# Kernel tuning notes

Measured on AMD Instinct MI355X. Metric: run time of the kernel, lower is better.

The kernel has to match this reference:

```python
import jax, jax.numpy as jnp
import numpy as np

N = 20000
E = 320000
R1 = 8        # num_rels (layer 1)
R2 = 256      # layer-2 num_rels == out_size (faithful to original positional-arg bug)
B = 8         # num_bases
D = 256       # hid_size == out_size
TIME_DIM = 2880
POI_DIM = 12
ROAD_DIM = 32


def relconv(h, src, dst, etype, coeff, bases, loop_w, bias):
    """DGL RelGraphConv with basis regularizer, sum aggregation, self-loop, bias.
    W_r = sum_b coeff[r,b] * bases[b]; msg_e = h[src_e] @ W_{etype_e}; agg = scatter-add to dst.
    Implemented memory-efficiently: project nodes into basis space once [B,N,D],
    then scan over the B bases (small fixed loop) for the gather/scale/scatter.
    """
    tb = jnp.einsum('nd,bdo->bno', h, bases)          # [B, N, D]
    c = coeff[etype]                                   # [E, B] per-edge basis coeffs

    def body(agg, xs):
        tb_b, c_b = xs                                 # [N,D], [E]
        msg = c_b[:, None] * tb_b[src]                 # [E, D]
        return agg + jax.ops.segment_sum(msg, dst, num_segments=N), None

    agg0 = jnp.zeros((N, bases.shape[-1]), h.dtype)
    agg, _ = jax.lax.scan(body, agg0, (tb, c.T))
    return agg + h @ loop_w + bias


def rgcn2(feat, src, dst, etype, c1, v1, l1, b1, c2, v2, l2, b2):
    h = relconv(feat, src, dst, etype, c1, v1, l1, b1)
    h = jax.nn.relu(h)  # dropout p=0.0 -> identity
    h = relconv(h, src, dst, etype, c2, v2, l2, b2)
    return h


def setup_inputs() -> dict:
    key = jax.random.key(0)
    ks = iter(jax.random.split(key, 48))
    f32 = jnp.float32

    def nrm(shape, std=0.02):
        return (jax.random.normal(next(ks), shape, dtype=f32) * std)

    inp = {
        'poi_distribution': jax.random.uniform(next(ks), (N, POI_DIM), dtype=f32),
        'time_distribution': jax.random.normal(next(ks), (N, TIME_DIM), dtype=f32),
        'road_feature': jax.random.normal(next(ks), (N, ROAD_DIM), dtype=f32),
        # input projections (torch Linear: stored here as [in,out])
        'W_poi': nrm((POI_DIM, 64)), 'b_poi': jnp.zeros((64,), f32),
        'W_time': nrm((TIME_DIM, 128)), 'b_time': jnp.zeros((128,), f32),
        'W_road': nrm((ROAD_DIM, 64)), 'b_road': jnp.zeros((64,), f32),
        # adj R-GCN layer params: coeff [R,B], bases [B,D,D], loop [D,D], bias [D]
        'a_coeff1': nrm((R1, B), 0.3), 'a_bases1': nrm((B, D, D)),
        'a_loop1': nrm((D, D)), 'a_bias1': jnp.zeros((D,), f32),
        'a_coeff2': nrm((R2, B), 0.3), 'a_bases2': nrm((B, D, D)),
        'a_loop2': nrm((D, D)), 'a_bias2': jnp.zeros((D,), f32),
        # no_adj R-GCN layer params
        'n_coeff1': nrm((R1, B), 0.3), 'n_bases1': nrm((B, D, D)),
        'n_loop1': nrm((D, D)), 'n_bias1': jnp.zeros((D,), f32),
        'n_coeff2': nrm((R2, B), 0.3), 'n_bases2': nrm((B, D, D)),
        'n_loop2': nrm((D, D)), 'n_bias2': jnp.zeros((D,), f32),
        # fusion
        'W_fuse': nrm((D, D)), 'b_fuse': jnp.zeros((D,), f32),
        'W_fuse_kg': nrm((D, D)), 'b_fuse_kg': jnp.zeros((D,), f32),
        # graphs (edge lists + relation types)
        'adj_src': jax.random.randint(next(ks), (E,), 0, N, dtype=jnp.int32),
        'adj_dst': jax.random.randint(next(ks), (E,), 0, N, dtype=jnp.int32),
        'adj_type': jax.random.randint(next(ks), (E,), 0, R1, dtype=jnp.int32),
        'no_adj_src': jax.random.randint(next(ks), (E,), 0, N, dtype=jnp.int32),
        'no_adj_dst': jax.random.randint(next(ks), (E,), 0, N, dtype=jnp.int32),
        'no_adj_type': jax.random.randint(next(ks), (E,), 0, R1, dtype=jnp.int32),
    }
    return inp


def reference(poi_distribution, time_distribution, road_feature,
              W_poi, b_poi, W_time, b_time, W_road, b_road,
              a_coeff1, a_bases1, a_loop1, a_bias1,
              a_coeff2, a_bases2, a_loop2, a_bias2,
              n_coeff1, n_bases1, n_loop1, n_bias1,
              n_coeff2, n_bases2, n_loop2, n_bias2,
              W_fuse, b_fuse, W_fuse_kg, b_fuse_kg,
              adj_src, adj_dst, adj_type,
              no_adj_src, no_adj_dst, no_adj_type):
    poi_feat = poi_distribution @ W_poi + b_poi       # [N, 64]
    time_feat = time_distribution @ W_time + b_time   # [N, 128]
    road_feat = road_feature @ W_road + b_road        # [N, 64]
    feat = jnp.concatenate([poi_feat, time_feat, road_feat], axis=1)  # [N, 256]

    adj_emb = rgcn2(feat, adj_src, adj_dst, adj_type,
                    a_coeff1, a_bases1, a_loop1, a_bias1,
                    a_coeff2, a_bases2, a_loop2, a_bias2)
    no_adj_emb = rgcn2(feat, no_adj_src, no_adj_dst, no_adj_type,
                       n_coeff1, n_bases1, n_loop1, n_bias1,
                       n_coeff2, n_bases2, n_loop2, n_bias2)

    fused = (adj_emb @ W_fuse + b_fuse) + (no_adj_emb @ W_fuse_kg + b_fuse_kg)
    return jax.nn.gelu(fused, approximate=False)      # torch nn.GELU is exact erf
```

## Files before the change

kernel.cpp:

```cpp
#include <hip/hip_runtime.h>
#include <math.h>

typedef unsigned short ushort_t;
typedef __bf16 bf16x8 __attribute__((ext_vector_type(8)));
typedef float  f32x4  __attribute__((ext_vector_type(4)));

constexpr int NN = 20000;
constexpr int EE = 320000;
constexpr int NC = 2304;
constexpr int TD = 2880;

__device__ __forceinline__ float b2f(ushort_t u) {
    return __uint_as_float(((unsigned int)u) << 16);
}
__device__ __forceinline__ ushort_t f2b(float f) {
    unsigned int u = __float_as_uint(f);
    u += 0x7fffu + ((u >> 16) & 1u);
    return (ushort_t)(u >> 16);
}
__device__ __forceinline__ float ldf(const void* p, size_t i, int f32m) {
    return f32m ? ((const float*)p)[i] : b2f(((const ushort_t*)p)[i]);
}
__device__ __forceinline__ void gl2lds16(const ushort_t* g, ushort_t* l) {
    __builtin_amdgcn_global_load_lds(
        (const __attribute__((address_space(1))) void*)g,
        (__attribute__((address_space(3))) void*)l, 16, 0, 0);
}

__device__ __forceinline__ void mfma_step(const ushort_t* As, const ushort_t* Bs,
                                          f32x4 (&acc)[4][4],
                                          int wm, int wn, int quad, int l16)
{
    bf16x8 afr[4], bfr[4];
#pragma unroll
    for (int mi = 0; mi < 4; mi++)
        afr[mi] = *(const bf16x8*)(As + (wm * 64 + mi * 16 + l16) * 32 + quad * 8);
#pragma unroll
    for (int ni = 0; ni < 4; ni++)
        bfr[ni] = *(const bf16x8*)(Bs + (wn * 64 + ni * 16 + l16) * 32 + quad * 8);
#pragma unroll
    for (int mi = 0; mi < 4; mi++)
#pragma unroll
        for (int ni = 0; ni < 4; ni++)
            acc[mi][ni] = __builtin_amdgcn_mfma_f32_16x16x32_bf16(
                afr[mi], bfr[ni], acc[mi][ni], 0, 0, 0);
}

__global__ void k_detect(const void* timeD, int* flags)
{
    __shared__ float mx[256];
    int t = threadIdx.x;
    float m = 0.f;
    for (int i = t; i < 1024; i += 256) {
        float v = fabsf(b2f(((const ushort_t*)timeD)[i]));
        if (!(v < 1e30f)) v = 1e30f;
        m = fmaxf(m, v);
    }
    mx[t] = m;
    __syncthreads();
    if (t == 0) {
        float mm = 0.f;
        for (int i = 0; i < 256; i++) mm = fmaxf(mm, mx[i]);
        flags[0] = (mm > 1e4f) ? 1 : 0;
        flags[1] = 0;
    }
}

__global__ void k_cvt16(const void* __restrict__ in, ushort_t* __restrict__ out,
                        int n, const int* __restrict__ mf)
{
    int f32m = mf[0];
    int i = blockIdx.x * 256 + threadIdx.x;
    if (i < n) out[i] = f32m ? f2b(((const float*)in)[i]) : ((const ushort_t*)in)[i];
}

__global__ __launch_bounds__(256) void gemm_bt(
    const ushort_t* __restrict__ A, int lda,
    const ushort_t* __restrict__ Bt, int ldb,
    void* __restrict__ C, int ldc, int col0, const int* __restrict__ of,
    const ushort_t* __restrict__ bias,
    int M, int Ncols, int K, int act)
{
    __shared__ ushort_t As[128 * 32];
    __shared__ ushort_t Bs[128 * 32];

    const int f32o = of[0];
    const int t    = threadIdx.x;
    const int wave = t >> 6, lane = t & 63;
    const int wm   = wave >> 1, wn = wave & 1;
    const int quad = lane >> 4, l16 = lane & 15;
    const int m0   = blockIdx.x * 128, n0 = blockIdx.y * 128;

    f32x4 acc[4][4];
#pragma unroll
    for (int i = 0; i < 4; i++)
#pragma unroll
        for (int j = 0; j < 4; j++) acc[i][j] = (f32x4){0.f, 0.f, 0.f, 0.f};

    for (int k0 = 0; k0 < K; k0 += 32) {
#pragma unroll
        for (int j = 0; j < 2; j++) {
            int c   = (wave * 2 + j) * 64 + lane;
            int row = c >> 2, kc = c & 3;
            ushort_t* ldsbase_a = As + (wave * 2 + j) * 512;
            ushort_t* ldsbase_b = Bs + (wave * 2 + j) * 512;
            gl2lds16(A  + (size_t)(m0 + row) * lda + k0 + kc * 8, ldsbase_a);
            gl2lds16(Bt + (size_t)(n0 + row) * ldb + k0 + kc * 8, ldsbase_b);
        }
        __syncthreads();
        mfma_step(As, Bs, acc, wm, wn, quad, l16);
        __syncthreads();
    }

#pragma unroll
    for (int mi = 0; mi < 4; mi++) {
#pragma unroll
        for (int r = 0; r < 4; r++) {
            int row = m0 + wm * 64 + mi * 16 + quad * 4 + r;
            if (row >= M) continue;
#pragma unroll
            for (int ni = 0; ni < 4; ni++) {
                int col = n0 + wn * 64 + ni * 16 + l16;
                float v = acc[mi][ni][r];
                if (bias) v += b2f(bias[col]);
                if (act == 1) v = fmaxf(v, 0.f);
                else if (act == 2) v = 0.5f * v * (1.f + erff(v * 0.70710678118654752f));
                size_t idx = (size_t)row * ldc + col0 + col;
                if (f32o) ((float*)C)[idx] = v;
                else      ((ushort_t*)C)[idx] = f2b(v);
            }
        }
    }
}

__global__ __launch_bounds__(256) void gemm_splitk(
    const void* __restrict__ A, int lda, const int* __restrict__ af,
    const ushort_t* __restrict__ Bt, int ldb,
    float* __restrict__ part, int M, int K, int KC)
{
    __shared__ ushort_t As[128 * 32];
    __shared__ ushort_t Bs[128 * 32];

    const int f32a = af[0];
    const int t    = threadIdx.x;
    const int wave = t >> 6, lane = t & 63;
    const int wm   = wave >> 1, wn = wave & 1;
    const int quad = lane >> 4, l16 = lane & 15;
    const int m0   = blockIdx.x * 128;
    const int kbeg = blockIdx.y * KC;
    const int kend = (kbeg + KC < K) ? kbeg + KC : K;

    f32x4 acc[4][4];
#pragma unroll
    for (int i = 0; i < 4; i++)
#pragma unroll
        for (int j = 0; j < 4; j++) acc[i][j] = (f32x4){0.f, 0.f, 0.f, 0.f};

    if (!f32a && (m0 + 128 <= M)) {
        const ushort_t* Ab = (const ushort_t*)A;
        for (int k0 = kbeg; k0 < kend; k0 += 32) {
#pragma unroll
            for (int j = 0; j < 2; j++) {
                int c   = (wave * 2 + j) * 64 + lane;
                int row = c >> 2, kc = c & 3;
                gl2lds16(Ab + (size_t)(m0 + row) * lda + k0 + kc * 8,
                         As + (wave * 2 + j) * 512);
                gl2lds16(Bt + (size_t)row * ldb + k0 + kc * 8,
                         Bs + (wave * 2 + j) * 512);
            }
            __syncthreads();
            mfma_step(As, Bs, acc, wm, wn, quad, l16);
            __syncthreads();
        }
    } else {
        for (int k0 = kbeg; k0 < kend; k0 += 32) {
#pragma unroll
            for (int i = 0; i < 2; i++) {
                int c = t + i * 256;
                int row = c >> 2, kc = c & 3;
                uint4 av = make_uint4(0, 0, 0, 0);
                int gr = m0 + row;
                if (gr < M) {
                    size_t base = (size_t)gr * lda + k0 + kc * 8;
                    if (f32a) {
                        const float* Af = (const float*)A + base;
                        float4 lo = *(const float4*)Af;
                        float4 hi = *(const float4*)(Af + 4);
                        av.x = (unsigned)f2b(lo.x) | ((unsigned)f2b(lo.y) << 16);
                        av.y = (unsigned)f2b(lo.z) | ((unsigned)f2b(lo.w) << 16);
                        av.z = (unsigned)f2b(hi.x) | ((unsigned)f2b(hi.y) << 16);
                        av.w = (unsigned)f2b(hi.z) | ((unsigned)f2b(hi.w) << 16);
                    } else {
                        av = *(const uint4*)((const ushort_t*)A + base);
                    }
                }
                *(uint4*)(As + row * 32 + kc * 8) = av;
                uint4 bv = *(const uint4*)(Bt + (size_t)row * ldb + k0 + kc * 8);
                *(uint4*)(Bs + row * 32 + kc * 8) = bv;
            }
            __syncthreads();
            mfma_step(As, Bs, acc, wm, wn, quad, l16);
            __syncthreads();
        }
    }

    float* dst = part + (size_t)blockIdx.y * ((size_t)M * 128);
#pragma unroll
    for (int mi = 0; mi < 4; mi++) {
#pragma unroll
        for (int r = 0; r < 4; r++) {
            int row = m0 + wm * 64 + mi * 16 + quad * 4 + r;
            if (row >= M) continue;
#pragma unroll
            for (int ni = 0; ni < 4; ni++) {
                int col = wn * 64 + ni * 16 + l16;
                dst[(size_t)row * 128 + col] = acc[mi][ni][r];
            }
        }
    }
}

__global__ void k_bias_time(const float* __restrict__ part, int nsplit,
                            const ushort_t* __restrict__ bt,
                            ushort_t* __restrict__ feat)
{
    int n = blockIdx.x, o = threadIdx.x;
    float a = b2f(bt[o]);
    for (int s = 0; s < nsplit; ++s)
        a += part[(size_t)s * NN * 128 + (size_t)n * 128 + o];
    feat[(size_t)n * 256 + 64 + o] = f2b(a);
}

__global__ void k_build_wcatT(const void* __restrict__ coeff,
                              const void* __restrict__ bases,
                              const void* __restrict__ loopw,
                              ushort_t* __restrict__ Wt, const int* __restrict__ mf)
{
    __shared__ ushort_t tile[32][33];
    int f32m = mf[0];
    int blk = blockIdx.x;
    int r = blk >> 6, kt = (blk >> 3) & 7, ot = blk & 7;
    int k0 = kt * 32, o0 = ot * 32;
    int oi = threadIdx.x & 31, k4 = threadIdx.x >> 5;
    float cf[8];
    if (r < 8) {
#pragma unroll
        for (int b = 0; b < 8; b++) cf[b] = ldf(coeff, r * 8 + b, f32m);
    }
#pragma unroll
    for (int p = 0; p < 4; ++p) {
        int ki = k4 * 4 + p, k = k0 + ki, o = o0 + oi;
        float acc;
        if (r == 8) {
            acc = ldf(loopw, (size_t)k * 256 + o, f32m);
        } else {
            acc = 0.f;
#pragma unroll
            for (int b = 0; b < 8; b++)
                acc += cf[b] * ldf(bases, ((size_t)b * 256 + k) * 256 + o, f32m);
        }
        tile[ki][oi] = f2b(acc);
    }
    __syncthreads();
    int ki2 = threadIdx.x & 31, o4 = threadIdx.x >> 5;
#pragma unroll
    for (int p = 0; p < 4; ++p) {
        int o2 = o4 * 4 + p;
        Wt[((size_t)(r * 256 + o0 + o2)) * 256 + k0 + ki2] = tile[ki2][o2];
    }
}

__global__ void k_trans32(const void* __restrict__ in, ushort_t* __restrict__ out,
                          int cols, int ldout, const int* __restrict__ mf)
{
    __shared__ ushort_t tile[32][33];
    int f32m = mf[0];
    int k0 = blockIdx.x * 32, o0 = blockIdx.y * 32;
    int oi = threadIdx.x & 31, k4 = threadIdx.x >> 5;
#pragma unroll
    for (int p = 0; p < 4; ++p) {
        int ki = k4 * 4 + p;
        tile[ki][oi] = f2b(ldf(in, (size_t)(k0 + ki) * cols + (o0 + oi), f32m));
    }
    __syncthreads();
    int ki2 = threadIdx.x & 31, o4 = threadIdx.x >> 5;
#pragma unroll
    for (int p = 0; p < 4; ++p) {
        int o2 = o4 * 4 + p;
        out[(size_t)(o0 + o2) * ldout + k0 + ki2] = tile[ki2][o2];
    }
}

__global__ void k_biasfuse(const void* __restrict__ bf, const void* __restrict__ bfk,
                           ushort_t* __restrict__ bias_cat, const int* __restrict__ mf)
{
    int f32m = mf[0];
    int o = threadIdx.x;
    bias_cat[o] = f2b(ldf(bf, o, f32m) + ldf(bfk, o, f32m));
}

__global__ void k_inproj(const void* __restrict__ poi, const void* __restrict__ Wp,
                         const void* __restrict__ bp,
                         const void* __restrict__ road, const void* __restrict__ Wr,
                         const void* __restrict__ br,
                         ushort_t* __restrict__ feat, const int* __restrict__ mf)
{
    int f32m = mf[0];
    int n = blockIdx.x, t = threadIdx.x;
    if (t < 64) {
        float a = ldf(bp, t, f32m);
#pragma unroll
        for (int k = 0; k < 12; k++)
            a += ldf(poi, (size_t)n * 12 + k, f32m) * ldf(Wp, k * 64 + t, f32m);
        feat[(size_t)n * 256 + t] = f2b(a);
    } else {
        int o = t - 64;
        float a = ldf(br, o, f32m);
#pragma unroll
        for (int k = 0; k < 32; k++)
            a += ldf(road, (size_t)n * 32 + k, f32m) * ldf(Wr, k * 64 + o, f32m);
        feat[(size_t)n * 256 + 192 + o] = f2b(a);
    }
}

__global__ void k_zero(int* __restrict__ p, int n)
{
    int i = blockIdx.x * 256 + threadIdx.x;
    if (i < n) p[i] = 0;
}
__global__ void k_count(const int* __restrict__ dst, int* __restrict__ deg, int e)
{
    int i = blockIdx.x * 256 + threadIdx.x;
    if (i < e) atomicAdd(&deg[dst[i]], 1);
}
__global__ void k_scan1(const int* __restrict__ deg, int* __restrict__ partial,
                        int* __restrict__ bsum, int n)
{
    int t = threadIdx.x, b = blockIdx.x;
    int i = b * 256 + t;
    int v = (i < n) ? deg[i] : 0;
    int lane = t & 63, w = t >> 6;
    int x = v;
#pragma unroll
    for (int d = 1; d < 64; d <<= 1) {
        int y = __shfl_up(x, d);
        if (lane >= d) x += y;
    }
    __shared__ int wt[4];
    if (lane == 63) wt[w] = x;
    __syncthreads();
    int woff = 0;
    for (int j = 0; j < 4; j++) if (j < w) woff += wt[j];
    int incl = x + woff;
    if (i < n) partial[i] = incl - v;
    if (t == 255) bsum[b] = incl;
}
__global__ void k_scan2(const int* __restrict__ bsum, int* __restrict__ boff, int nb)
{
    int t = threadIdx.x;
    int v = (t < nb) ? bsum[t] : 0;
    int lane = t & 63, w = t >> 6;
    int x = v;
#pragma unroll
    for (int d = 1; d < 64; d <<= 1) {
        int y = __shfl_up(x, d);
        if (lane >= d) x += y;
    }
    __shared__ int wt[4];
    if (lane == 63) wt[w] = x;
    __syncthreads();
    int woff = 0;
    for (int j = 0; j < 4; j++) if (j < w) woff += wt[j];
    boff[t] = (x + woff) - v;
}
__global__ void k_scan3(const int* __restrict__ boff, int* __restrict__ rs,
                        int* __restrict__ cur, int n)
{
    int i = blockIdx.x * 256 + threadIdx.x;
    if (i < n) {
        int v = rs[i] + boff[blockIdx.x];
        rs[i] = v;
        cur[i] = v;
    }
}
__global__ void k_fill(const int* __restrict__ src, const int* __restrict__ dst,
                       const int* __restrict__ et, int* __restrict__ cur,
                       int* __restrict__ sorted, int e)
{
    int i = blockIdx.x * 256 + threadIdx.x;
    if (i < e) {
        int pos = atomicAdd(&cur[dst[i]], 1);
        sorted[pos] = (src[i] << 3) | et[i];
    }
}

__global__ __launch_bounds__(256) void k_agg_full(
    const ushort_t* __restrict__ tb,
    const int* __restrict__ rs, const int* __restrict__ deg,
    const int* __restrict__ sorted, const ushort_t* __restrict__ bias,
    ushort_t* __restrict__ out, int ldo, int col0, int act, int n_nodes)
{
    int w = blockIdx.x * 4 + (threadIdx.x >> 6);
    if (w >= n_nodes) return;
    int lane = threadIdx.x & 63;
    int lo = lane * 4;

    float a0 = b2f(bias[lo + 0]);
    float a1 = b2f(bias[lo + 1]);
    float a2 = b2f(bias[lo + 2]);
    float a3 = b2f(bias[lo + 3]);
    {
        ushort4 lv = *(const ushort4*)(tb + (size_t)w * NC + 8 * 256 + lo);
        a0 += b2f(lv.x); a1 += b2f(lv.y); a2 += b2f(lv.z); a3 += b2f(lv.w);
    }
    int s = rs[w], cnt = deg[w];
    int j = 0;
    for (; j + 4 <= cnt; j += 4) {
        int p0 = sorted[s + j + 0];
        int p1 = sorted[s + j + 1];
        int p2 = sorted[s + j + 2];
        int p3 = sorted[s + j + 3];
        ushort4 v0 = *(const ushort4*)(tb + ((size_t)(p0 >> 3) * 9 + (p0 & 7)) * 256 + lo);
        ushort4 v1 = *(const ushort4*)(tb + ((size_t)(p1 >> 3) * 9 + (p1 & 7)) * 256 + lo);
        ushort4 v2 = *(const ushort4*)(tb + ((size_t)(p2 >> 3) * 9 + (p2 & 7)) * 256 + lo);
        ushort4 v3 = *(const ushort4*)(tb + ((size_t)(p3 >> 3) * 9 + (p3 & 7)) * 256 + lo);
        a0 += b2f(v0.x); a1 += b2f(v0.y); a2 += b2f(v0.z); a3 += b2f(v0.w);
        a0 += b2f(v1.x); a1 += b2f(v1.y); a2 += b2f(v1.z); a3 += b2f(v1.w);
        a0 += b2f(v2.x); a1 += b2f(v2.y); a2 += b2f(v2.z); a3 += b2f(v2.w);
        a0 += b2f(v3.x); a1 += b2f(v3.y); a2 += b2f(v3.z); a3 += b2f(v3.w);
    }
    for (; j < cnt; ++j) {
        int p = sorted[s + j];
        ushort4 v = *(const ushort4*)(tb + ((size_t)(p >> 3) * 9 + (p & 7)) * 256 + lo);
        a0 += b2f(v.x); a1 += b2f(v.y); a2 += b2f(v.z); a3 += b2f(v.w);
    }
    if (act) {
        a0 = fmaxf(a0, 0.f); a1 = fmaxf(a1, 0.f);
        a2 = fmaxf(a2, 0.f); a3 = fmaxf(a3, 0.f);
    }
    ushort4 o;
    o.x = f2b(a0); o.y = f2b(a1); o.z = f2b(a2); o.w = f2b(a3);
    *(ushort4*)(out + (size_t)w * ldo + col0 + lo) = o;
}

__global__ __launch_bounds__(256) void k_agg2(
    const ushort_t* __restrict__ tb, int ldt,
    const int* __restrict__ rs, const int* __restrict__ deg,
    const int* __restrict__ sorted, const ushort_t* __restrict__ bias,
    float* __restrict__ accf, ushort_t* __restrict__ out,
    int ldo, int col0, int act, int b0, int b1, int flags, int n_nodes)
{
    int w = blockIdx.x * 4 + (threadIdx.x >> 6);
    if (w >= n_nodes) return;
    int lane = threadIdx.x & 63;

    float a0, a1, a2, a3;
    if (flags & 1) {
        a0 = b2f(bias[lane * 4 + 0]);
        a1 = b2f(bias[lane * 4 + 1]);
        a2 = b2f(bias[lane * 4 + 2]);
        a3 = b2f(bias[lane * 4 + 3]);
    } else {
        float4 v = *(const float4*)(accf + (size_t)w * 256 + lane * 4);
        a0 = v.x; a1 = v.y; a2 = v.z; a3 = v.w;
    }
    if (b0 <= 8 && 8 < b1) {
        ushort4 lv = *(const ushort4*)(tb + (size_t)w * ldt + (8 - b0) * 256 + lane * 4);
        a0 += b2f(lv.x); a1 += b2f(lv.y); a2 += b2f(lv.z); a3 += b2f(lv.w);
    }
    int s = rs[w], cnt = deg[w];
    for (int j = 0; j < cnt; ++j) {
        int p = sorted[s + j];
        int r = p & 7;
        if (r >= b0 && r < b1) {
            const ushort_t* q = tb + (size_t)(p >> 3) * ldt + (r - b0) * 256 + lane * 4;
            ushort4 v = *(const ushort4*)q;
            a0 += b2f(v.x); a1 += b2f(v.y); a2 += b2f(v.z); a3 += b2f(v.w);
        }
    }
    if (flags & 2) {
        if (act) {
            a0 = fmaxf(a0, 0.f); a1 = fmaxf(a1, 0.f);
            a2 = fmaxf(a2, 0.f); a3 = fmaxf(a3, 0.f);
        }
        ushort4 o;
        o.x = f2b(a0); o.y = f2b(a1); o.z = f2b(a2); o.w = f2b(a3);
        *(ushort4*)(out + (size_t)w * ldo + col0 + lane * 4) = o;
    } else {
        *(float4*)(accf + (size_t)w * 256 + lane * 4) = make_float4(a0, a1, a2, a3);
    }
}

extern "C" void kernel_launch(void* const* d_in, const int* in_sizes, int n_in,
                              void* d_out, int out_size, void* d_ws, size_t ws_size,
                              hipStream_t stream)
{
    const void* poi    = d_in[0];
    const void* timeD  = d_in[1];
    const void* roadF  = d_in[2];
    const void* W_poi  = d_in[3];
    const void* b_poi  = d_in[4];
    const void* W_time = d_in[5];
    const void* b_time = d_in[6];
    const void* W_road = d_in[7];
    const void* b_road = d_in[8];
    const void* W_fuse  = d_in[25];
    const void* b_fuse  = d_in[26];
    const void* W_fusek = d_in[27];
    const void* b_fusek = d_in[28];
    const int* g_src[2] = {(const int*)d_in[29], (const int*)d_in[32]};
    const int* g_dst[2] = {(const int*)d_in[30], (const int*)d_in[33]};
    const int* g_typ[2] = {(const int*)d_in[31], (const int*)d_in[34]};

    char* p = (char*)d_ws;
    auto alloc = [&](size_t bytes) -> char* {
        char* r = p;
        p += (bytes + 255) & ~(size_t)255;
        return r;
    };
    int*      flags   = (int*)alloc(2 * 4);
    ushort_t* feat    = (ushort_t*)alloc((size_t)NN * 256 * 2);
    ushort_t* h1      = (ushort_t*)alloc((size_t)NN * 256 * 2);
    ushort_t* fused   = (ushort_t*)alloc((size_t)NN * 512 * 2);
    float*    accf    = (float*)alloc((size_t)NN * 256 * 4);
    ushort_t* wcat    = (ushort_t*)alloc((size_t)NC * 256 * 2);
    ushort_t* wtt     = (ushort_t*)alloc((size_t)128 * TD * 2);
    ushort_t* wft     = (ushort_t*)alloc((size_t)256 * 512 * 2);
    ushort_t* biascat = (ushort_t*)alloc(256 * 2);
    ushort_t* btws    = (ushort_t*)alloc(128 * 2);
    ushort_t* biws    = (ushort_t*)alloc(256 * 2);
    int* deg    = (int*)alloc((size_t)NN * 4);
    int* rs     = (int*)alloc((size_t)NN * 4);
    int* cur    = (int*)alloc((size_t)NN * 4);
    int* sorted = (int*)alloc((size_t)EE * 4);
    int* bsum   = (int*)alloc(256 * 4);
    int* boff   = (int*)alloc(256 * 4);

    size_t psl       = (size_t)NN * 128 * 4;
    size_t per_block = (size_t)NN * 256 * 2;
    size_t used0 = (size_t)(p - (char*)d_ws);
    int SPLITS;
    float* tpart;
    if (ws_size > used0 + per_block + 512 + psl) {
        size_t s = (ws_size - used0 - per_block - 512) / psl;
        SPLITS = (int)(s > 6 ? 6 : s);
        tpart  = (float*)alloc(psl * SPLITS);
    } else {
        tpart  = accf;
        SPLITS = 2;
    }
    const int KC = TD / SPLITS;

    size_t used = (size_t)(p - (char*)d_ws);
    int C = 1;
    if (ws_size > used + 512) {
        size_t c = (ws_size - used - 512) / per_block;
        C = (c < 1) ? 1 : (c > 9 ? 9 : (int)c);
    }
    ushort_t* tbuf = (ushort_t*)alloc(per_block * C);
    const int nch = (9 + C - 1) / C;

    const int SB = (NN + 255) / 256;
    const int EB = (EE + 255) / 256;
    const int MT = (NN + 127) / 128;

    k_detect<<<1, 256, 0, stream>>>(timeD, flags);
    k_trans32<<<dim3(TD / 32, 128 / 32), 256, 0, stream>>>(W_time, wtt, 128, TD, flags);
    k_trans32<<<dim3(8, 8), 256, 0, stream>>>(W_fuse, wft, 256, 512, flags);
    k_trans32<<<dim3(8, 8), 256, 0, stream>>>(W_fusek, wft + 256, 256, 512, flags);
    k_biasfuse<<<1, 256, 0, stream>>>(b_fuse, b_fusek, biascat, flags);
    k_cvt16<<<1, 256, 0, stream>>>(b_time, btws, 128, flags);

    k_inproj<<<NN, 128, 0, stream>>>(poi, W_poi, b_poi, roadF, W_road, b_road,
                                     feat, flags);
    gemm_splitk<<<dim3(MT, SPLITS), 256, 0, stream>>>(timeD, TD, flags, wtt, TD,
                                                      tpart, NN, TD, KC);
    k_bias_time<<<NN, 128, 0, stream>>>(tpart, SPLITS, btws, feat);

    for (int g = 0; g < 2; ++g) {
        k_zero<<<SB, 256, 0, stream>>>(deg, NN);
        k_count<<<EB, 256, 0, stream>>>(g_dst[g], deg, EE);
        k_scan1<<<SB, 256, 0, stream>>>(deg, rs, bsum, NN);
        k_scan2<<<1, 256, 0, stream>>>(bsum, boff, SB);
        k_scan3<<<SB, 256, 0, stream>>>(boff, rs, cur, NN);
        k_fill<<<EB, 256, 0, stream>>>(g_src[g], g_dst[g], g_typ[g], cur, sorted, EE);

        for (int l = 0; l < 2; ++l) {
            int rc = g * 2 + l;
            const void* cf  = d_in[9 + rc * 4 + 0];
            const void* bs_ = d_in[9 + rc * 4 + 1];
            const void* lw  = d_in[9 + rc * 4 + 2];
            const void* bi  = d_in[9 + rc * 4 + 3];
            k_build_wcatT<<<9 * 64, 256, 0, stream>>>(cf, bs_, lw, wcat, flags);
            k_cvt16<<<1, 256, 0, stream>>>(bi, biws, 256, flags);
            const ushort_t* Ain = (l == 0) ? feat : h1;
            ushort_t* dest = (l == 0) ? h1 : fused;
            int ldo  = (l == 0) ? 256 : 512;
            int col0 = (l == 0) ? 0 : g * 256;
            int act  = (l == 0) ? 1 : 0;
            if (nch == 1) {
                gemm_bt<<<dim3(MT, 18), 256, 0, stream>>>(
                    Ain, 256, wcat, 256, tbuf, NC, 0, flags + 1, nullptr,
                    NN, NC, 256, 0);
                k_agg_full<<<NN / 4, 256, 0, stream>>>(tbuf, rs, deg, sorted,
                                                       biws, dest, ldo, col0,
                                                       act, NN);
            } else {
                for (int c = 0; c < nch; ++c) {
                    int b0 = c * C;
                    int b1 = (b0 + C < 9) ? b0 + C : 9;
                    int nb = b1 - b0;
                    gemm_bt<<<dim3(MT, nb * 2), 256, 0, stream>>>(
                        Ain, 256, wcat + (size_t)b0 * 256 * 256, 256,
                        tbuf, nb * 256, 0, flags + 1, nullptr, NN, nb * 256, 256, 0);
                    int fl = (c == 0 ? 1 : 0) | (c == nch - 1 ? 2 : 0);
                    k_agg2<<<NN / 4, 256, 0, stream>>>(tbuf, nb * 256, rs, deg, sorted,
                                                       biws, accf, dest, ldo, col0, act,
                                                       b0, b1, fl, NN);
                }
            }
        }
    }

    gemm_bt<<<dim3(MT, 2), 256, 0, stream>>>(fused, 512, wft, 512,
                                             d_out, 256, 0, flags, biascat,
                                             NN, 256, 512, 2);
}
```

Baseline: 1.009 ms.

## Merge both graphs' layer-1 GEMMs and remap GEMM tiles across XCDs

Layer 1 of both R-GCNs shares the same input features, so their concatenated basis weights are now run through one wider GEMM into a doubled transform buffer, provided the workspace is large enough. The aggregation kernel gains a stride and column base so it can read either half. Per-graph CSR buffers are kept separately so both graphs can be sorted up front. The GEMM also remaps flat block IDs so consecutive tiles land on the same XCD, for better L2 reuse of the shared A/B tiles. The cost is a larger workspace requirement, and if the workspace is too small it falls back to the old path.

```diff
diff --git a/kernel.cpp b/kernel.cpp
--- a/kernel.cpp
+++ b/kernel.cpp
@@ -89,7 +89,15 @@
     const int wave = t >> 6, lane = t & 63;
     const int wm   = wave >> 1, wn = wave & 1;
     const int quad = lane >> 4, l16 = lane & 15;
-    const int m0   = blockIdx.x * 128, n0 = blockIdx.y * 128;
+
+    const int NBx = gridDim.x, NBy = gridDim.y;
+    const int total = NBx * NBy;
+    const int flat  = blockIdx.y * NBx + blockIdx.x;
+    const int xcd = flat & 7, i8 = flat >> 3;
+    const int q = total >> 3, r = total & 7;
+    const int pos = (xcd < r) ? xcd * (q + 1) + i8
+                              : r * (q + 1) + (xcd - r) * q + i8;
+    const int m0 = (pos / NBy) * 128, n0 = (pos % NBy) * 128;
 
     f32x4 acc[4][4];
 #pragma unroll
@@ -115,13 +123,13 @@
 #pragma unroll
     for (int mi = 0; mi < 4; mi++) {
 #pragma unroll
-        for (int r = 0; r < 4; r++) {
-            int row = m0 + wm * 64 + mi * 16 + quad * 4 + r;
+        for (int r2 = 0; r2 < 4; r2++) {
+            int row = m0 + wm * 64 + mi * 16 + quad * 4 + r2;
             if (row >= M) continue;
 #pragma unroll
             for (int ni = 0; ni < 4; ni++) {
                 int col = n0 + wn * 64 + ni * 16 + l16;
-                float v = acc[mi][ni][r];
+                float v = acc[mi][ni][r2];
                 if (bias) v += b2f(bias[col]);
                 if (act == 1) v = fmaxf(v, 0.f);
                 else if (act == 2) v = 0.5f * v * (1.f + erff(v * 0.70710678118654752f));
@@ -395,7 +403,7 @@
 }
 
 __global__ __launch_bounds__(256) void k_agg_full(
-    const ushort_t* __restrict__ tb,
+    const ushort_t* __restrict__ tb, int ldt, int colbase,
     const int* __restrict__ rs, const int* __restrict__ deg,
     const int* __restrict__ sorted, const ushort_t* __restrict__ bias,
     ushort_t* __restrict__ out, int ldo, int col0, int act, int n_nodes)
@@ -404,13 +412,14 @@
     if (w >= n_nodes) return;
     int lane = threadIdx.x & 63;
     int lo = lane * 4;
+    const ushort_t* tbb = tb + colbase + lo;
 
     float a0 = b2f(bias[lo + 0]);
     float a1 = b2f(bias[lo + 1]);
     float a2 = b2f(bias[lo + 2]);
     float a3 = b2f(bias[lo + 3]);
     {
-        ushort4 lv = *(const ushort4*)(tb + (size_t)w * NC + 8 * 256 + lo);
+        ushort4 lv = *(const ushort4*)(tbb + (size_t)w * ldt + 2048);
         a0 += b2f(lv.x); a1 += b2f(lv.y); a2 += b2f(lv.z); a3 += b2f(lv.w);
     }
     int s = rs[w], cnt = deg[w];
@@ -420,10 +429,10 @@
         int p1 = sorted[s + j + 1];
         int p2 = sorted[s + j + 2];
         int p3 = sorted[s + j + 3];
-        ushort4 v0 = *(const ushort4*)(tb + ((size_t)(p0 >> 3) * 9 + (p0 & 7)) * 256 + lo);
-        ushort4 v1 = *(const ushort4*)(tb + ((size_t)(p1 >> 3) * 9 + (p1 & 7)) * 256 + lo);
-        ushort4 v2 = *(const ushort4*)(tb + ((size_t)(p2 >> 3) * 9 + (p2 & 7)) * 256 + lo);
-        ushort4 v3 = *(const ushort4*)(tb + ((size_t)(p3 >> 3) * 9 + (p3 & 7)) * 256 + lo);
+        ushort4 v0 = *(const ushort4*)(tbb + (size_t)(p0 >> 3) * ldt + (p0 & 7) * 256);
+        ushort4 v1 = *(const ushort4*)(tbb + (size_t)(p1 >> 3) * ldt + (p1 & 7) * 256);
+        ushort4 v2 = *(const ushort4*)(tbb + (size_t)(p2 >> 3) * ldt + (p2 & 7) * 256);
+        ushort4 v3 = *(const ushort4*)(tbb + (size_t)(p3 >> 3) * ldt + (p3 & 7) * 256);
         a0 += b2f(v0.x); a1 += b2f(v0.y); a2 += b2f(v0.z); a3 += b2f(v0.w);
         a0 += b2f(v1.x); a1 += b2f(v1.y); a2 += b2f(v1.z); a3 += b2f(v1.w);
         a0 += b2f(v2.x); a1 += b2f(v2.y); a2 += b2f(v2.z); a3 += b2f(v2.w);
@@ -431,7 +440,7 @@
     }
     for (; j < cnt; ++j) {
         int p = sorted[s + j];
-        ushort4 v = *(const ushort4*)(tb + ((size_t)(p >> 3) * 9 + (p & 7)) * 256 + lo);
+        ushort4 v = *(const ushort4*)(tbb + (size_t)(p >> 3) * ldt + (p & 7) * 256);
         a0 += b2f(v.x); a1 += b2f(v.y); a2 += b2f(v.z); a3 += b2f(v.w);
     }
     if (act) {
@@ -520,23 +529,28 @@
     };
     int*      flags   = (int*)alloc(2 * 4);
     ushort_t* feat    = (ushort_t*)alloc((size_t)NN * 256 * 2);
-    ushort_t* h1      = (ushort_t*)alloc((size_t)NN * 256 * 2);
+    ushort_t* h1a     = (ushort_t*)alloc((size_t)NN * 256 * 2);
+    ushort_t* h1b     = (ushort_t*)alloc((size_t)NN * 256 * 2);
     ushort_t* fused   = (ushort_t*)alloc((size_t)NN * 512 * 2);
     float*    accf    = (float*)alloc((size_t)NN * 256 * 4);
-    ushort_t* wcat    = (ushort_t*)alloc((size_t)NC * 256 * 2);
+    ushort_t* wcat    = (ushort_t*)alloc((size_t)2 * NC * 256 * 2);
     ushort_t* wtt     = (ushort_t*)alloc((size_t)128 * TD * 2);
     ushort_t* wft     = (ushort_t*)alloc((size_t)256 * 512 * 2);
     ushort_t* biascat = (ushort_t*)alloc(256 * 2);
     ushort_t* btws    = (ushort_t*)alloc(128 * 2);
-    ushort_t* biws    = (ushort_t*)alloc(256 * 2);
-    int* deg    = (int*)alloc((size_t)NN * 4);
-    int* rs     = (int*)alloc((size_t)NN * 4);
-    int* cur    = (int*)alloc((size_t)NN * 4);
-    int* sorted = (int*)alloc((size_t)EE * 4);
-    int* bsum   = (int*)alloc(256 * 4);
-    int* boff   = (int*)alloc(256 * 4);
+    ushort_t* biws0   = (ushort_t*)alloc(256 * 2);
+    ushort_t* biws1   = (ushort_t*)alloc(256 * 2);
+    int* deg[2]; int* rs[2]; int* sorted[2];
+    deg[0] = (int*)alloc((size_t)NN * 4);  deg[1] = (int*)alloc((size_t)NN * 4);
+    rs[0]  = (int*)alloc((size_t)NN * 4);  rs[1]  = (int*)alloc((size_t)NN * 4);
+    sorted[0] = (int*)alloc((size_t)EE * 4);
+    sorted[1] = (int*)alloc((size_t)EE * 4);
+    int* cur  = (int*)alloc((size_t)NN * 4);
+    int* bsum = (int*)alloc(256 * 4);
+    int* boff = (int*)alloc(256 * 4);
 
     size_t psl       = (size_t)NN * 128 * 4;
+    size_t per_tb    = (size_t)NN * NC * 2;
     size_t per_block = (size_t)NN * 256 * 2;
     size_t used0 = (size_t)(p - (char*)d_ws);
     int SPLITS;
@@ -552,12 +566,18 @@
     const int KC = TD / SPLITS;
 
     size_t used = (size_t)(p - (char*)d_ws);
-    int C = 1;
-    if (ws_size > used + 512) {
-        size_t c = (ws_size - used - 512) / per_block;
-        C = (c < 1) ? 1 : (c > 9 ? 9 : (int)c);
-    }
-    ushort_t* tbuf = (ushort_t*)alloc(per_block * C);
+    int MERGED = 0, C = 1;
+    ushort_t* tbuf;
+    if (ws_size > used + 2 * per_tb + 512) {
+        MERGED = 1;
+        tbuf = (ushort_t*)alloc(2 * per_tb);
+    } else {
+        if (ws_size > used + 512) {
+            size_t c = (ws_size - used - 512) / per_block;
+            C = (c < 1) ? 1 : (c > 9 ? 9 : (int)c);
+        }
+        tbuf = (ushort_t*)alloc(per_block * C);
+    }
     const int nch = (9 + C - 1) / C;
 
     const int SB = (NN + 255) / 256;
@@ -578,45 +598,80 @@
     k_bias_time<<<NN, 128, 0, stream>>>(tpart, SPLITS, btws, feat);
 
     for (int g = 0; g < 2; ++g) {
-        k_zero<<<SB, 256, 0, stream>>>(deg, NN);
-        k_count<<<EB, 256, 0, stream>>>(g_dst[g], deg, EE);
-        k_scan1<<<SB, 256, 0, stream>>>(deg, rs, bsum, NN);
+        k_zero<<<SB, 256, 0, stream>>>(deg[g], NN);
+        k_count<<<EB, 256, 0, stream>>>(g_dst[g], deg[g], EE);
+        k_scan1<<<SB, 256, 0, stream>>>(deg[g], rs[g], bsum, NN);
         k_scan2<<<1, 256, 0, stream>>>(bsum, boff, SB);
-        k_scan3<<<SB, 256, 0, stream>>>(boff, rs, cur, NN);
-        k_fill<<<EB, 256, 0, stream>>>(g_src[g], g_dst[g], g_typ[g], cur, sorted, EE);
-
-        for (int l = 0; l < 2; ++l) {
-            int rc = g * 2 + l;
-            const void* cf  = d_in[9 + rc * 4 + 0];
-            const void* bs_ = d_in[9 + rc * 4 + 1];
-            const void* lw  = d_in[9 + rc * 4 + 2];
-            const void* bi  = d_in[9 + rc * 4 + 3];
-            k_build_wcatT<<<9 * 64, 256, 0, stream>>>(cf, bs_, lw, wcat, flags);
-            k_cvt16<<<1, 256, 0, stream>>>(bi, biws, 256, flags);
-            const ushort_t* Ain = (l == 0) ? feat : h1;
-            ushort_t* dest = (l == 0) ? h1 : fused;
-            int ldo  = (l == 0) ? 256 : 512;
-            int col0 = (l == 0) ? 0 : g * 256;
-            int act  = (l == 0) ? 1 : 0;
-            if (nch == 1) {
-                gemm_bt<<<dim3(MT, 18), 256, 0, stream>>>(
-                    Ain, 256, wcat, 256, tbuf, NC, 0, flags + 1, nullptr,
-                    NN, NC, 256, 0);
-                k_agg_full<<<NN / 4, 256, 0, stream>>>(tbuf, rs, deg, sorted,
-                                                       biws, dest, ldo, col0,
-                                                       act, NN);
-            } else {
-                for (int c = 0; c < nch; ++c) {
-                    int b0 = c * C;
-                    int b1 = (b0 + C < 9) ? b0 + C : 9;
-                    int nb = b1 - b0;
-                    gemm_bt<<<dim3(MT, nb * 2), 256, 0, stream>>>(
-                        Ain, 256, wcat + (size_t)b0 * 256 * 256, 256,
-                        tbuf, nb * 256, 0, flags + 1, nullptr, NN, nb * 256, 256, 0);
-                    int fl = (c == 0 ? 1 : 0) | (c == nch - 1 ? 2 : 0);
-                    k_agg2<<<NN / 4, 256, 0, stream>>>(tbuf, nb * 256, rs, deg, sorted,
-                                                       biws, accf, dest, ldo, col0, act,
-                                                       b0, b1, fl, NN);
+        k_scan3<<<SB, 256, 0, stream>>>(boff, rs[g], cur, NN);
+        k_fill<<<EB, 256, 0, stream>>>(g_src[g], g_dst[g], g_typ[g], cur,
+                                       sorted[g], EE);
+    }
+
+    if (MERGED) {
+        k_build_wcatT<<<9 * 64, 256, 0, stream>>>(d_in[9], d_in[10], d_in[11],
+                                                  wcat, flags);
+        k_build_wcatT<<<9 * 64, 256, 0, stream>>>(d_in[17], d_in[18], d_in[19],
+                                                  wcat + (size_t)NC * 256, flags);
+        k_cvt16<<<1, 256, 0, stream>>>(d_in[12], biws0, 256, flags);
+        k_cvt16<<<1, 256, 0, stream>>>(d_in[20], biws1, 256, flags);
+        gemm_bt<<<dim3(MT, 36), 256, 0, stream>>>(
+            feat, 256, wcat, 256, tbuf, 2 * NC, 0, flags + 1, nullptr,
+            NN, 2 * NC, 256, 0);
+        k_agg_full<<<NN / 4, 256, 0, stream>>>(tbuf, 2 * NC, 0, rs[0], deg[0],
+                                               sorted[0], biws0, h1a, 256, 0, 1, NN);
+        k_agg_full<<<NN / 4, 256, 0, stream>>>(tbuf, 2 * NC, NC, rs[1], deg[1],
+                                               sorted[1], biws1, h1b, 256, 0, 1, NN);
+        for (int g = 0; g < 2; ++g) {
+            int base = (g == 0) ? 13 : 21;
+            k_build_wcatT<<<9 * 64, 256, 0, stream>>>(d_in[base], d_in[base + 1],
+                                                      d_in[base + 2], wcat, flags);
+            k_cvt16<<<1, 256, 0, stream>>>(d_in[base + 3], biws0, 256, flags);
+            const ushort_t* Ain = (g == 0) ? h1a : h1b;
+            gemm_bt<<<dim3(MT, 18), 256, 0, stream>>>(
+                Ain, 256, wcat, 256, tbuf, NC, 0, flags + 1, nullptr,
+                NN, NC, 256, 0);
+            k_agg_full<<<NN / 4, 256, 0, stream>>>(tbuf, NC, 0, rs[g], deg[g],
+                                                   sorted[g], biws0, fused, 512,
+                                                   g * 256, 0, NN);
+        }
+    } else {
+        for (int g = 0; g < 2; ++g) {
+            for (int l = 0; l < 2; ++l) {
+                int rc = g * 2 + l;
+                const void* cf  = d_in[9 + rc * 4 + 0];
+                const void* bs_ = d_in[9 + rc * 4 + 1];
+                const void* lw  = d_in[9 + rc * 4 + 2];
+                const void* bi  = d_in[9 + rc * 4 + 3];
+                k_build_wcatT<<<9 * 64, 256, 0, stream>>>(cf, bs_, lw, wcat, flags);
+                k_cvt16<<<1, 256, 0, stream>>>(bi, biws0, 256, flags);
+                const ushort_t* Ain = (l == 0) ? feat : h1a;
+                ushort_t* dest = (l == 0) ? h1a : fused;
+                int ldo  = (l == 0) ? 256 : 512;
+                int col0 = (l == 0) ? 0 : g * 256;
+                int act  = (l == 0) ? 1 : 0;
+                if (nch == 1) {
+                    gemm_bt<<<dim3(MT, 18), 256, 0, stream>>>(
+                        Ain, 256, wcat, 256, tbuf, NC, 0, flags + 1, nullptr,
+                        NN, NC, 256, 0);
+                    k_agg_full<<<NN / 4, 256, 0, stream>>>(tbuf, NC, 0, rs[g],
+                                                           deg[g], sorted[g],
+                                                           biws0, dest, ldo, col0,
+                                                           act, NN);
+                } else {
+                    for (int c = 0; c < nch; ++c) {
+                        int b0 = c * C;
+                        int b1 = (b0 + C < 9) ? b0 + C : 9;
+                        int nb = b1 - b0;
+                        gemm_bt<<<dim3(MT, nb * 2), 256, 0, stream>>>(
+                            Ain, 256, wcat + (size_t)b0 * 256 * 256, 256,
+                            tbuf, nb * 256, 0, flags + 1, nullptr, NN, nb * 256,
+                            256, 0);
+                        int fl = (c == 0 ? 1 : 0) | (c == nch - 1 ? 2 : 0);
+                        k_agg2<<<NN / 4, 256, 0, stream>>>(tbuf, nb * 256, rs[g],
+                                                           deg[g], sorted[g],
+                                                           biws0, accf, dest, ldo,
+                                                           col0, act, b0, b1, fl, NN);
+                    }
                 }
             }
         }
```

Measured after the change: 983.8 us. -2.5%, faster.
